# Kernel optimization log

Hardware: AMD Instinct MI355X
Metric: run time of the kernel (lower is better)

The kernel has to match this reference:

```python
import jax, jax.numpy as jnp
import numpy as np

EPS = 1e-5  # nn.LayerNorm default
HIDDENS = 1024

def layer_norm(x, gamma, beta):
    mu = jnp.mean(x, axis=-1, keepdims=True)
    var = jnp.var(x, axis=-1, keepdims=True)  # biased, as in torch LayerNorm
    return (x - mu) * jax.lax.rsqrt(var + EPS) * gamma + beta

def setup_inputs() -> dict:
    key = jax.random.key(0)
    kX, kY, kK, kQ = jax.random.split(key, 4)
    B, S, F, H = 8, 2048, 1024, HIDDENS
    X = jax.random.normal(kX, (B, S, F), dtype=jnp.float32)
    Y = jax.random.normal(kY, (B, S, F), dtype=jnp.float32)
    K = jax.random.normal(kK, (F, H), dtype=jnp.float32)
    Q = jax.random.normal(kQ, (F, H), dtype=jnp.float32)
    g1 = jnp.ones((H,), dtype=jnp.float32)
    b1 = jnp.zeros((H,), dtype=jnp.float32)
    g2 = jnp.ones((H,), dtype=jnp.float32)
    b2 = jnp.zeros((H,), dtype=jnp.float32)
    return {"X": X, "Y": Y, "K": K, "Q": Q, "g1": g1, "b1": b1, "g2": g2, "b2": b2}

def reference(X, Y, K, Q, g1, b1, g2, b2):
    keys = layer_norm(Y @ K, g1, b1)          # [B,S,H]
    queries = layer_norm(X @ Q, g2, b2)       # [B,S,H]
    alpha = jnp.einsum('bqh,bkh->bqk', queries, keys) / HIDDENS  # [B,S,S]
    alpha = jax.nn.softmax(alpha, axis=2)
    return jnp.einsum('bqk,bkf->bqf', alpha, Y)  # values are raw Y
```

## Files before the change

kernel.cpp:

```cpp
#include <hip/hip_runtime.h>
#include <hip/hip_bf16.h>
#include <stdint.h>

typedef __attribute__((ext_vector_type(8))) short bf16x8;
typedef __attribute__((ext_vector_type(4))) float f32x4;

#define GLB_AS __attribute__((address_space(1)))
#define LDS_AS __attribute__((address_space(3)))

__device__ __forceinline__ void g2l16(const void* g, void* l) {
  __builtin_amdgcn_global_load_lds((const GLB_AS void*)g, (LDS_AS void*)l, 16, 0, 0);
}

__device__ __forceinline__ unsigned short f2bf(float f) {
  union { __hip_bfloat16 h; unsigned short u; } cv;
  cv.h = __float2bfloat16(f);
  return cv.u;
}
__device__ __forceinline__ float bf2f(unsigned int u) {
  return __uint_as_float(u << 16);
}

#define BM 128
#define BN 128
#define BKG 64

template <int OUT_BF16>
__global__ __launch_bounds__(256)
void gemm_bt(const unsigned short* __restrict__ A,
             const unsigned short* __restrict__ Bt,
             void* __restrict__ C,
             int K, int lda, int ldb, int ldc,
             long long sA, long long sB, long long sC,
             float scale, int gx, int gy)
{
  __shared__ __attribute__((aligned(16))) short As[BM * BKG];
  __shared__ __attribute__((aligned(16))) short Bs[BN * BKG];

  const int nwg = gridDim.x;
  const int bid = blockIdx.x;
  const int wgid = (bid & 7) * (nwg >> 3) + (bid >> 3);
  const int tx = wgid % gx;
  const int rest = wgid / gx;
  const int ty = rest % gy;
  const int tz = rest / gy;

  const int tid = threadIdx.x;
  const unsigned short* Ab = A + (long long)tz * sA + (long long)ty * BM * lda;
  const unsigned short* Bb = Bt + (long long)tz * sB + (long long)tx * BN * ldb;

  const int lane = tid & 63, wid = tid >> 6;
  const int wr = wid >> 1, wc = wid & 1;
  const int l15 = lane & 15, l4 = lane >> 4;

  f32x4 acc[4][4];
#pragma unroll
  for (int i = 0; i < 4; ++i)
#pragma unroll
    for (int j = 0; j < 4; ++j) acc[i][j] = f32x4{0.f, 0.f, 0.f, 0.f};

  const unsigned short* gAp[4];
  const unsigned short* gBp[4];
#pragma unroll
  for (int i = 0; i < 4; ++i) {
    int c = i * 256 + tid;
    int row = c >> 3, slot = c & 7;
    int gslot = slot ^ (row & 7);
    gAp[i] = Ab + (long long)row * lda + gslot * 8;
    gBp[i] = Bb + (long long)row * ldb + gslot * 8;
  }

  const int kTiles = K / BKG;
  for (int kt = 0; kt < kTiles; ++kt) {
    __syncthreads();
#pragma unroll
    for (int i = 0; i < 4; ++i)
      g2l16(gAp[i] + kt * BKG, (char*)As + i * 4096 + tid * 16);
#pragma unroll
    for (int i = 0; i < 4; ++i)
      g2l16(gBp[i] + kt * BKG, (char*)Bs + i * 4096 + tid * 16);
    __syncthreads();

#pragma unroll
    for (int h = 0; h < 2; ++h) {
      bf16x8 af[4], bfr[4];
#pragma unroll
      for (int fr = 0; fr < 4; ++fr) {
        int row = wr * 64 + fr * 16 + l15;
        int slot = (h * 4 + l4) ^ (row & 7);
        af[fr] = *(const bf16x8*)((const char*)As + row * 128 + slot * 16);
      }
#pragma unroll
      for (int fc = 0; fc < 4; ++fc) {
        int row = wc * 64 + fc * 16 + l15;
        int slot = (h * 4 + l4) ^ (row & 7);
        bfr[fc] = *(const bf16x8*)((const char*)Bs + row * 128 + slot * 16);
      }
#pragma unroll
      for (int fr = 0; fr < 4; ++fr)
#pragma unroll
        for (int fc = 0; fc < 4; ++fc)
          acc[fr][fc] = __builtin_amdgcn_mfma_f32_16x16x32_bf16(
              af[fr], bfr[fc], acc[fr][fc], 0, 0, 0);
    }
  }

  const long long m0 = (long long)ty * BM + wr * 64;
  const long long n0 = (long long)tx * BN + wc * 64;
  if (OUT_BF16) {
    unsigned short* Cc = (unsigned short*)C + (long long)tz * sC;
#pragma unroll
    for (int fr = 0; fr < 4; ++fr)
#pragma unroll
      for (int fc = 0; fc < 4; ++fc)
#pragma unroll
        for (int i = 0; i < 4; ++i) {
          long long r = m0 + fr * 16 + l4 * 4 + i;
          long long col = n0 + fc * 16 + l15;
          Cc[r * ldc + col] = f2bf(acc[fr][fc][i] * scale);
        }
  } else {
    float* Cf = (float*)C + (long long)tz * sC;
#pragma unroll
    for (int fr = 0; fr < 4; ++fr)
#pragma unroll
      for (int fc = 0; fc < 4; ++fc)
#pragma unroll
        for (int i = 0; i < 4; ++i) {
          long long r = m0 + fr * 16 + l4 * 4 + i;
          long long col = n0 + fc * 16 + l15;
          Cf[r * ldc + col] = acc[fr][fc][i];
        }
  }
}

__global__ __launch_bounds__(256)
void ln_bf16(const float* __restrict__ in, unsigned short* __restrict__ out,
             const float* __restrict__ g, const float* __restrict__ b)
{
  const long long row = blockIdx.x;
  const int t = threadIdx.x;
  const float4 v = ((const float4*)(in + row * 1024))[t];
  float s = v.x + v.y + v.z + v.w;
  float ss = v.x * v.x + v.y * v.y + v.z * v.z + v.w * v.w;
#pragma unroll
  for (int o = 32; o >= 1; o >>= 1) {
    s += __shfl_xor(s, o);
    ss += __shfl_xor(ss, o);
  }
  __shared__ float red[8];
  if ((t & 63) == 0) { red[t >> 6] = s; red[4 + (t >> 6)] = ss; }
  __syncthreads();
  s = red[0] + red[1] + red[2] + red[3];
  ss = red[4] + red[5] + red[6] + red[7];
  const float mean = s * (1.f / 1024.f);
  const float var = ss * (1.f / 1024.f) - mean * mean;
  const float rs = rsqrtf(var + 1e-5f);
  const float4 gv = ((const float4*)g)[t];
  const float4 bv = ((const float4*)b)[t];
  ushort4 o4;
  o4.x = f2bf((v.x - mean) * rs * gv.x + bv.x);
  o4.y = f2bf((v.y - mean) * rs * gv.y + bv.y);
  o4.z = f2bf((v.z - mean) * rs * gv.z + bv.z);
  o4.w = f2bf((v.w - mean) * rs * gv.w + bv.w);
  ((ushort4*)(out + row * 1024))[t] = o4;
}

__global__ __launch_bounds__(256)
void softmax_bf16(unsigned short* __restrict__ a)
{
  const long long row = blockIdx.x;
  unsigned short* p = a + row * 2048;
  const int t = threadIdx.x;
  uint4 pk = ((const uint4*)p)[t];
  float v[8];
  v[0] = bf2f(pk.x & 0xffffu); v[1] = bf2f(pk.x >> 16);
  v[2] = bf2f(pk.y & 0xffffu); v[3] = bf2f(pk.y >> 16);
  v[4] = bf2f(pk.z & 0xffffu); v[5] = bf2f(pk.z >> 16);
  v[6] = bf2f(pk.w & 0xffffu); v[7] = bf2f(pk.w >> 16);

  float m = v[0];
#pragma unroll
  for (int i = 1; i < 8; ++i) m = fmaxf(m, v[i]);
#pragma unroll
  for (int o = 32; o >= 1; o >>= 1) m = fmaxf(m, __shfl_xor(m, o));
  __shared__ float redm[4];
  if ((t & 63) == 0) redm[t >> 6] = m;
  __syncthreads();
  m = fmaxf(fmaxf(redm[0], redm[1]), fmaxf(redm[2], redm[3]));

  float e[8];
  float s = 0.f;
#pragma unroll
  for (int i = 0; i < 8; ++i) { e[i] = __expf(v[i] - m); s += e[i]; }
#pragma unroll
  for (int o = 32; o >= 1; o >>= 1) s += __shfl_xor(s, o);
  __shared__ float reds[4];
  if ((t & 63) == 0) reds[t >> 6] = s;
  __syncthreads();
  s = reds[0] + reds[1] + reds[2] + reds[3];
  const float inv = 1.f / s;

  pk.x = (unsigned int)f2bf(e[0] * inv) | ((unsigned int)f2bf(e[1] * inv) << 16);
  pk.y = (unsigned int)f2bf(e[2] * inv) | ((unsigned int)f2bf(e[3] * inv) << 16);
  pk.z = (unsigned int)f2bf(e[4] * inv) | ((unsigned int)f2bf(e[5] * inv) << 16);
  pk.w = (unsigned int)f2bf(e[6] * inv) | ((unsigned int)f2bf(e[7] * inv) << 16);
  ((uint4*)p)[t] = pk;
}

__global__ __launch_bounds__(256)
void cast_flat(const float* __restrict__ in, unsigned short* __restrict__ out, int n4)
{
  int idx = blockIdx.x * 256 + threadIdx.x;
  const int stride = gridDim.x * 256;
  for (; idx < n4; idx += stride) {
    float4 v = ((const float4*)in)[idx];
    ushort4 o;
    o.x = f2bf(v.x); o.y = f2bf(v.y); o.z = f2bf(v.z); o.w = f2bf(v.w);
    ((ushort4*)out)[idx] = o;
  }
}

__global__ __launch_bounds__(256)
void transpose_cast(const float* __restrict__ in, unsigned short* __restrict__ out,
                    int R, int C)
{
  __shared__ float tile[32][33];
  const int z = blockIdx.z;
  const float* src = in + (long long)z * R * C;
  unsigned short* dst = out + (long long)z * R * C;
  const int tx = threadIdx.x, ty = threadIdx.y;
  const int c0 = blockIdx.x * 32, r0 = blockIdx.y * 32;
#pragma unroll
  for (int k = 0; k < 4; ++k)
    tile[ty + 8 * k][tx] = src[(long long)(r0 + ty + 8 * k) * C + c0 + tx];
  __syncthreads();
#pragma unroll
  for (int k = 0; k < 4; ++k)
    dst[(long long)(c0 + ty + 8 * k) * R + r0 + tx] = f2bf(tile[tx][ty + 8 * k]);
}

extern "C" void kernel_launch(void* const* d_in, const int* in_sizes, int n_in,
                              void* d_out, int out_size, void* d_ws, size_t ws_size,
                              hipStream_t stream)
{
  const float* X = (const float*)d_in[0];
  const float* Y = (const float*)d_in[1];
  const float* Kw = (const float*)d_in[2];
  const float* Qw = (const float*)d_in[3];
  const float* g1 = (const float*)d_in[4];
  const float* b1 = (const float*)d_in[5];
  const float* g2 = (const float*)d_in[6];
  const float* b2 = (const float*)d_in[7];
  float* out = (float*)d_out;

  char* ws = (char*)d_ws;
  float* tempf = (float*)ws;
  unsigned short* alpha = (unsigned short*)ws;
  unsigned short* keys = (unsigned short*)(ws + (64ll << 20));
  unsigned short* xb   = (unsigned short*)(ws + (96ll << 20));
  unsigned short* ybq  = (unsigned short*)(ws + (128ll << 20));
  unsigned short* yt   = (unsigned short*)(ws + (160ll << 20));
  unsigned short* ktw  = (unsigned short*)(ws + (192ll << 20));
  unsigned short* qtw  = (unsigned short*)(ws + (194ll << 20));

  const int n4 = 16777216 / 4;

  cast_flat<<<2048, 256, 0, stream>>>(Y, ybq, n4);
  cast_flat<<<2048, 256, 0, stream>>>(X, xb, n4);
  transpose_cast<<<dim3(32, 32, 1), dim3(32, 8), 0, stream>>>(Kw, ktw, 1024, 1024);
  transpose_cast<<<dim3(32, 32, 1), dim3(32, 8), 0, stream>>>(Qw, qtw, 1024, 1024);
  transpose_cast<<<dim3(32, 64, 8), dim3(32, 8), 0, stream>>>(Y, yt, 2048, 1024);

  gemm_bt<0><<<1024, 256, 0, stream>>>(
      ybq, ktw, tempf, 1024, 1024, 1024, 1024, 0, 0, 0, 1.f, 8, 128);
  ln_bf16<<<16384, 256, 0, stream>>>(tempf, keys, g1, b1);

  gemm_bt<0><<<1024, 256, 0, stream>>>(
      xb, qtw, tempf, 1024, 1024, 1024, 1024, 0, 0, 0, 1.f, 8, 128);
  ln_bf16<<<16384, 256, 0, stream>>>(tempf, ybq, g2, b2);

  gemm_bt<1><<<2048, 256, 0, stream>>>(
      ybq, keys, alpha, 1024, 1024, 1024, 2048,
      2048ll * 1024, 2048ll * 1024, 2048ll * 2048, 1.f / 1024.f, 16, 16);

  softmax_bf16<<<16384, 256, 0, stream>>>(alpha);

  gemm_bt<0><<<1024, 256, 0, stream>>>(
      alpha, yt, out, 2048, 2048, 2048, 1024,
      2048ll * 2048, 1024ll * 2048, 2048ll * 1024, 1.f, 8, 16);
}
```

Measured before the change: 546.7 us.

## Replace GEMM with 256x256-tile, 4-stage pipelined 512-thread kernel

Replaces the 128x128 single-buffered GEMM with a 256x256-tile kernel of 8 waves. It streams K in 32-wide slices through a 4-slot LDS ring using async global-to-LDS loads, split into A and B halves, with explicit vmcnt waits, barriers and MFMA priority raising. The aim is to hide global load latency behind MFMA work and to raise data reuse per tile. The cost is 128KB of LDS per workgroup and fewer workgroups (256 or 512) on a large chip. That may underfill the CUs and limit occupancy, and a pipelining error could cause races.

```diff
diff --git a/kernel.cpp b/kernel.cpp
--- a/kernel.cpp
+++ b/kernel.cpp
@@ -21,115 +21,156 @@
   return __uint_as_float(u << 16);
 }
 
-#define BM 128
-#define BN 128
-#define BKG 64
-
 template <int OUT_BF16>
-__global__ __launch_bounds__(256)
-void gemm_bt(const unsigned short* __restrict__ A,
+__global__ __launch_bounds__(512, 2)
+void gemm256(const unsigned short* __restrict__ A,
              const unsigned short* __restrict__ Bt,
              void* __restrict__ C,
              int K, int lda, int ldb, int ldc,
              long long sA, long long sB, long long sC,
              float scale, int gx, int gy)
 {
-  __shared__ __attribute__((aligned(16))) short As[BM * BKG];
-  __shared__ __attribute__((aligned(16))) short Bs[BN * BKG];
+  __shared__ __attribute__((aligned(16))) char lds[131072];
 
   const int nwg = gridDim.x;
   const int bid = blockIdx.x;
   const int wgid = (bid & 7) * (nwg >> 3) + (bid >> 3);
-  const int tx = wgid % gx;
+  const int bx = wgid % gx;
   const int rest = wgid / gx;
-  const int ty = rest % gy;
-  const int tz = rest / gy;
+  const int by = rest % gy;
+  const int bz = rest / gy;
 
   const int tid = threadIdx.x;
-  const unsigned short* Ab = A + (long long)tz * sA + (long long)ty * BM * lda;
-  const unsigned short* Bb = Bt + (long long)tz * sB + (long long)tx * BN * ldb;
-
   const int lane = tid & 63, wid = tid >> 6;
-  const int wr = wid >> 1, wc = wid & 1;
+  const int wr = wid >> 2, wc = wid & 3;
   const int l15 = lane & 15, l4 = lane >> 4;
 
-  f32x4 acc[4][4];
-#pragma unroll
-  for (int i = 0; i < 4; ++i)
-#pragma unroll
-    for (int j = 0; j < 4; ++j) acc[i][j] = f32x4{0.f, 0.f, 0.f, 0.f};
-
-  const unsigned short* gAp[4];
-  const unsigned short* gBp[4];
-#pragma unroll
-  for (int i = 0; i < 4; ++i) {
-    int c = i * 256 + tid;
-    int row = c >> 3, slot = c & 7;
-    int gslot = slot ^ (row & 7);
-    gAp[i] = Ab + (long long)row * lda + gslot * 8;
-    gBp[i] = Bb + (long long)row * ldb + gslot * 8;
+  const unsigned short* Ab = A + (long long)bz * sA + (long long)by * 256 * lda;
+  const unsigned short* Bb = Bt + (long long)bz * sB + (long long)bx * 256 * ldb;
+
+  const int c0 = tid, c1 = 512 + tid;
+  const int r0 = c0 >> 2, q0 = ((c0 & 3) - r0) & 3;
+  const int r1 = c1 >> 2, q1 = ((c1 & 3) - r1) & 3;
+  const unsigned short* gA0 = Ab + (long long)r0 * lda + q0 * 8;
+  const unsigned short* gA1 = Ab + (long long)r1 * lda + q1 * 8;
+  const unsigned short* gB0 = Bb + (long long)r0 * ldb + q0 * 8;
+  const unsigned short* gB1 = Bb + (long long)r1 * ldb + q1 * 8;
+  const int dc0 = c0 * 16, dc1 = c1 * 16;
+
+#define STAGE_A(slot_, kt_)                                        \
+  do {                                                             \
+    char* base_ = lds + (slot_) * 32768;                           \
+    g2l16(gA0 + (kt_) * 32, base_ + dc0);                          \
+    g2l16(gA1 + (kt_) * 32, base_ + dc1);                          \
+  } while (0)
+#define STAGE_B(slot_, kt_)                                        \
+  do {                                                             \
+    char* base_ = lds + (slot_) * 32768 + 16384;                   \
+    g2l16(gB0 + (kt_) * 32, base_ + dc0);                          \
+    g2l16(gB1 + (kt_) * 32, base_ + dc1);                          \
+  } while (0)
+
+  f32x4 acc[8][4];
+#pragma unroll
+  for (int m = 0; m < 8; ++m)
+#pragma unroll
+    for (int n = 0; n < 4; ++n) acc[m][n] = f32x4{0.f, 0.f, 0.f, 0.f};
+
+  const int nst = K / 32;
+
+  STAGE_A(0, 0); STAGE_B(0, 0);
+  STAGE_A(1, 1); STAGE_B(1, 1);
+  STAGE_A(2, 2); STAGE_B(2, 2);
+  asm volatile("s_waitcnt vmcnt(8)" ::: "memory");
+  __builtin_amdgcn_sched_barrier(0);
+  __builtin_amdgcn_s_barrier();
+  __builtin_amdgcn_sched_barrier(0);
+
+  bf16x8 a[8], b[4];
+  for (int t = 0; t < nst; ++t) {
+    const int s = t & 3;
+    const char* sbA = lds + s * 32768;
+    const char* sbB = sbA + 16384;
+
+#pragma unroll
+    for (int m = 0; m < 4; ++m) {
+      int r = wr * 128 + m * 16 + l15;
+      a[m] = *(const bf16x8*)(sbA + r * 64 + (((l4 + r) & 3) << 4));
+    }
+#pragma unroll
+    for (int n = 0; n < 4; ++n) {
+      int r = wc * 64 + n * 16 + l15;
+      b[n] = *(const bf16x8*)(sbB + r * 64 + (((l4 + r) & 3) << 4));
+    }
+    if (t + 3 < nst) STAGE_A((t + 3) & 3, t + 3);
+    __builtin_amdgcn_sched_barrier(0);
+    __builtin_amdgcn_s_barrier();
+    __builtin_amdgcn_sched_barrier(0);
+    __builtin_amdgcn_s_setprio(1);
+#pragma unroll
+    for (int m = 0; m < 4; ++m)
+#pragma unroll
+      for (int n = 0; n < 4; ++n)
+        acc[m][n] = __builtin_amdgcn_mfma_f32_16x16x32_bf16(a[m], b[n], acc[m][n], 0, 0, 0);
+    __builtin_amdgcn_s_setprio(0);
+    __builtin_amdgcn_sched_barrier(0);
+    __builtin_amdgcn_s_barrier();
+    __builtin_amdgcn_sched_barrier(0);
+
+#pragma unroll
+    for (int m = 4; m < 8; ++m) {
+      int r = wr * 128 + m * 16 + l15;
+      a[m] = *(const bf16x8*)(sbA + r * 64 + (((l4 + r) & 3) << 4));
+    }
+    if (t + 3 < nst) STAGE_B((t + 3) & 3, t + 3);
+    __builtin_amdgcn_sched_barrier(0);
+    __builtin_amdgcn_s_barrier();
+    __builtin_amdgcn_sched_barrier(0);
+    __builtin_amdgcn_s_setprio(1);
+#pragma unroll
+    for (int m = 4; m < 8; ++m)
+#pragma unroll
+      for (int n = 0; n < 4; ++n)
+        acc[m][n] = __builtin_amdgcn_mfma_f32_16x16x32_bf16(a[m], b[n], acc[m][n], 0, 0, 0);
+    __builtin_amdgcn_s_setprio(0);
+    if (t + 1 < nst) {
+      int f = nst - 1 - t; if (f > 3) f = 3;
+      if (f == 3)      asm volatile("s_waitcnt vmcnt(8)" ::: "memory");
+      else if (f == 2) asm volatile("s_waitcnt vmcnt(4)" ::: "memory");
+      else             asm volatile("s_waitcnt vmcnt(0)" ::: "memory");
+    }
+    __builtin_amdgcn_sched_barrier(0);
+    __builtin_amdgcn_s_barrier();
+    __builtin_amdgcn_sched_barrier(0);
   }
-
-  const int kTiles = K / BKG;
-  for (int kt = 0; kt < kTiles; ++kt) {
-    __syncthreads();
-#pragma unroll
-    for (int i = 0; i < 4; ++i)
-      g2l16(gAp[i] + kt * BKG, (char*)As + i * 4096 + tid * 16);
-#pragma unroll
-    for (int i = 0; i < 4; ++i)
-      g2l16(gBp[i] + kt * BKG, (char*)Bs + i * 4096 + tid * 16);
-    __syncthreads();
-
-#pragma unroll
-    for (int h = 0; h < 2; ++h) {
-      bf16x8 af[4], bfr[4];
-#pragma unroll
-      for (int fr = 0; fr < 4; ++fr) {
-        int row = wr * 64 + fr * 16 + l15;
-        int slot = (h * 4 + l4) ^ (row & 7);
-        af[fr] = *(const bf16x8*)((const char*)As + row * 128 + slot * 16);
-      }
-#pragma unroll
-      for (int fc = 0; fc < 4; ++fc) {
-        int row = wc * 64 + fc * 16 + l15;
-        int slot = (h * 4 + l4) ^ (row & 7);
-        bfr[fc] = *(const bf16x8*)((const char*)Bs + row * 128 + slot * 16);
-      }
-#pragma unroll
-      for (int fr = 0; fr < 4; ++fr)
-#pragma unroll
-        for (int fc = 0; fc < 4; ++fc)
-          acc[fr][fc] = __builtin_amdgcn_mfma_f32_16x16x32_bf16(
-              af[fr], bfr[fc], acc[fr][fc], 0, 0, 0);
-    }
-  }
-
-  const long long m0 = (long long)ty * BM + wr * 64;
-  const long long n0 = (long long)tx * BN + wc * 64;
+#undef STAGE_A
+#undef STAGE_B
+
+  const long long m0 = (long long)by * 256 + wr * 128;
+  const long long n0 = (long long)bx * 256 + wc * 64;
   if (OUT_BF16) {
-    unsigned short* Cc = (unsigned short*)C + (long long)tz * sC;
-#pragma unroll
-    for (int fr = 0; fr < 4; ++fr)
-#pragma unroll
-      for (int fc = 0; fc < 4; ++fc)
+    unsigned short* Cc = (unsigned short*)C + (long long)bz * sC;
+#pragma unroll
+    for (int m = 0; m < 8; ++m)
+#pragma unroll
+      for (int n = 0; n < 4; ++n)
 #pragma unroll
         for (int i = 0; i < 4; ++i) {
-          long long r = m0 + fr * 16 + l4 * 4 + i;
-          long long col = n0 + fc * 16 + l15;
-          Cc[r * ldc + col] = f2bf(acc[fr][fc][i] * scale);
+          long long r = m0 + m * 16 + l4 * 4 + i;
+          long long col = n0 + n * 16 + l15;
+          Cc[r * ldc + col] = f2bf(acc[m][n][i] * scale);
         }
   } else {
-    float* Cf = (float*)C + (long long)tz * sC;
-#pragma unroll
-    for (int fr = 0; fr < 4; ++fr)
-#pragma unroll
-      for (int fc = 0; fc < 4; ++fc)
+    float* Cf = (float*)C + (long long)bz * sC;
+#pragma unroll
+    for (int m = 0; m < 8; ++m)
+#pragma unroll
+      for (int n = 0; n < 4; ++n)
 #pragma unroll
         for (int i = 0; i < 4; ++i) {
-          long long r = m0 + fr * 16 + l4 * 4 + i;
-          long long col = n0 + fc * 16 + l15;
-          Cf[r * ldc + col] = acc[fr][fc][i];
+          long long r = m0 + m * 16 + l4 * 4 + i;
+          long long col = n0 + n * 16 + l15;
+          Cf[r * ldc + col] = acc[m][n][i];
         }
   }
 }
@@ -272,21 +313,21 @@
   transpose_cast<<<dim3(32, 32, 1), dim3(32, 8), 0, stream>>>(Qw, qtw, 1024, 1024);
   transpose_cast<<<dim3(32, 64, 8), dim3(32, 8), 0, stream>>>(Y, yt, 2048, 1024);
 
-  gemm_bt<0><<<1024, 256, 0, stream>>>(
-      ybq, ktw, tempf, 1024, 1024, 1024, 1024, 0, 0, 0, 1.f, 8, 128);
+  gemm256<0><<<256, 512, 0, stream>>>(
+      ybq, ktw, tempf, 1024, 1024, 1024, 1024, 0, 0, 0, 1.f, 4, 64);
   ln_bf16<<<16384, 256, 0, stream>>>(tempf, keys, g1, b1);
 
-  gemm_bt<0><<<1024, 256, 0, stream>>>(
-      xb, qtw, tempf, 1024, 1024, 1024, 1024, 0, 0, 0, 1.f, 8, 128);
+  gemm256<0><<<256, 512, 0, stream>>>(
+      xb, qtw, tempf, 1024, 1024, 1024, 1024, 0, 0, 0, 1.f, 4, 64);
   ln_bf16<<<16384, 256, 0, stream>>>(tempf, ybq, g2, b2);
 
-  gemm_bt<1><<<2048, 256, 0, stream>>>(
+  gemm256<1><<<512, 512, 0, stream>>>(
       ybq, keys, alpha, 1024, 1024, 1024, 2048,
-      2048ll * 1024, 2048ll * 1024, 2048ll * 2048, 1.f / 1024.f, 16, 16);
+      2048ll * 1024, 2048ll * 1024, 2048ll * 2048, 1.f / 1024.f, 8, 8);
 
   softmax_bf16<<<16384, 256, 0, stream>>>(alpha);
 
-  gemm_bt<0><<<1024, 256, 0, stream>>>(
+  gemm256<0><<<256, 512, 0, stream>>>(
       alpha, yt, out, 2048, 2048, 2048, 1024,
-      2048ll * 2048, 1024ll * 2048, 2048ll * 1024, 1.f, 8, 16);
-}
+      2048ll * 2048, 1024ll * 2048, 2048ll * 1024, 1.f, 4, 8);
+}
```

Result: faster. 494.2 us (-9.6%).
